# Kernel tuning notes

Hardware: AMD Instinct MI355X
Metric: run time of the kernel (lower is better)

The kernel has to match this reference:

```python
import jax, jax.numpy as jnp
import numpy as np

NUM_LAYERS = 3
NUM_NODES = 120000  # num_users + num_items
LATENT_DIM = 64
NUM_EDGES = 2000000


def setup_inputs() -> dict:
    key = jax.random.key(0)
    k1, k2 = jax.random.split(key)
    edge_index = jax.random.randint(k1, (2, NUM_EDGES), 0, NUM_NODES, dtype=jnp.int64 if jax.config.jax_enable_x64 else jnp.int32)
    # init_parameters: normal(std=0.1) for LightGCN
    emb_weight = jax.random.normal(k2, (NUM_NODES, LATENT_DIM), dtype=jnp.float32) * 0.1
    return {"edge_index": edge_index, "emb_weight": emb_weight}


def reference(edge_index, emb_weight):
    """RecSysGNN (model='LightGCN') forward. Returns (emb0, out)."""
    n = emb_weight.shape[0]
    src, dst = edge_index[0], edge_index[1]
    # degree of target nodes (degree(to_, x.size(0)))
    deg = jax.ops.segment_sum(jnp.ones(src.shape[0], dtype=emb_weight.dtype), dst, num_segments=n)
    deg_inv_sqrt = jnp.where(deg > 0, jax.lax.rsqrt(jnp.maximum(deg, 1.0)), 0.0)
    norm = deg_inv_sqrt[src] * deg_inv_sqrt[dst]  # [E]

    emb0 = emb_weight
    emb = emb0
    acc = emb0  # running sum of layer embeddings for final mean
    for _ in range(NUM_LAYERS):
        msg = norm[:, None] * emb[src]                      # [E, d] gather + scale
        emb = jax.ops.segment_sum(msg, dst, num_segments=n)  # scatter-add to targets
        acc = acc + emb
    out = acc / (NUM_LAYERS + 1)  # mean over stacked [emb0, emb1, ..., embL]
    return (emb0, out)
```

## Files before the change

kernel.cpp:

```cpp
#include <hip/hip_runtime.h>


#define DIM 64
#define BN 512
#define BSH 9
#define CHUNK 4096

typedef unsigned short u16;
typedef unsigned int u32;

static __device__ __forceinline__ float bf2f_lo(u32 p) { return __uint_as_float(p << 16); }
static __device__ __forceinline__ float bf2f_hi(u32 p) { return __uint_as_float(p & 0xffff0000u); }
static __device__ __forceinline__ u16 f2bf(float f) {
    unsigned u = __float_as_uint(f);
    return (u16)((u + 0x7fffu + ((u >> 16) & 1u)) >> 16);
}
static __device__ __forceinline__ u32 pack2(float a, float b) {
    return (u32)f2bf(a) | ((u32)f2bf(b) << 16);
}

__global__ void zero_cur(int* __restrict__ cursor) { cursor[threadIdx.x] = 0; }

__global__ void __launch_bounds__(512) c1_scatter(
        const int* __restrict__ src, const int* __restrict__ dst,
        int* __restrict__ cursor, u32* __restrict__ slab, int E, int CAP) {
    __shared__ u32 buf[CHUNK];
    __shared__ unsigned char bb[CHUNK];
    __shared__ int posb[256], startb[256], gbase[256];
    int w = blockIdx.x, tid = threadIdx.x;
    int lo = w * CHUNK, hi = min(lo + CHUNK, E);
    if (tid < 256) posb[tid] = 0;
    __syncthreads();
    for (int i = lo + tid; i < hi; i += 512) atomicAdd(&posb[dst[i] >> BSH], 1);
    __syncthreads();
    int x = 0;
    if (tid < 256) {
        x = posb[tid];
        gbase[tid] = x ? atomicAdd(cursor + tid, x) : 0;
    }
    __syncthreads();
    for (int off = 1; off < 256; off <<= 1) {
        int t = (tid >= off && tid < 256) ? posb[tid - off] : 0;
        __syncthreads();
        if (tid < 256) posb[tid] += t;
        __syncthreads();
    }
    if (tid < 256) startb[tid] = posb[tid] - x;
    __syncthreads();
    if (tid < 256) posb[tid] = startb[tid];
    __syncthreads();
    for (int i = lo + tid; i < hi; i += 512) {
        int d = dst[i], b = d >> BSH;
        int q = atomicAdd(&posb[b], 1);
        buf[q] = ((u32)src[i] << BSH) | (u32)(d & (BN - 1));
        bb[q] = (unsigned char)b;
    }
    __syncthreads();
    int n = hi - lo;
    for (int q = tid; q < n; q += 512) {
        int b = bb[q];
        slab[(size_t)b * CAP + gbase[b] + (q - startb[b])] = buf[q];
    }
}

__global__ void __launch_bounds__(512) c3_build(
        const u32* __restrict__ slab, const int* __restrict__ cursor,
        int* __restrict__ col, int2* __restrict__ row_se, float* __restrict__ dis,
        int N, int CAP, int NB) {
    __shared__ int cur[BN];
    __shared__ int ps[512];
    int b = blockIdx.x, tid = threadIdx.x;
    int xc = (tid < NB) ? cursor[tid] : 0;
    if (tid < 256) ps[tid] = xc;
    __syncthreads();
    for (int off = 1; off < 256; off <<= 1) {
        int t = (tid >= off && tid < 256) ? ps[tid - off] : 0;
        __syncthreads();
        if (tid < 256) ps[tid] += t;
        __syncthreads();
    }
    int lo  = b ? ps[b - 1] : 0;
    int cnt = cursor[b];
    __syncthreads();

    int nodeBase = b << BSH;
    int nLoc = min(BN, N - nodeBase);
    const u32* sp = slab + (size_t)b * CAP;
    cur[tid] = 0;
    __syncthreads();
    for (int i = tid; i < cnt; i += 512) atomicAdd(&cur[sp[i] & (BN - 1)], 1);
    __syncthreads();
    int c0 = cur[tid];
    ps[tid] = c0;
    __syncthreads();
    for (int off = 1; off < 512; off <<= 1) {
        int t = (tid >= off) ? ps[tid - off] : 0;
        __syncthreads();
        ps[tid] += t;
        __syncthreads();
    }
    int base = ps[tid] - c0;
    cur[tid] = base;
    if (tid < nLoc) {
        dis[nodeBase + tid] = c0 ? rsqrtf((float)c0) : 0.f;
        row_se[nodeBase + tid] = make_int2(lo + base, lo + base + c0);
    }
    __syncthreads();
    for (int i = tid; i < cnt; i += 512) {
        u32 v = sp[i];
        int q = atomicAdd(&cur[v & (BN - 1)], 1);
        col[lo + q] = (int)(v >> BSH);
    }
}

__global__ void cvt_copy(const float4* __restrict__ emb, const float* __restrict__ dis,
                         ushort4* __restrict__ e0b, float4* __restrict__ emb0_out, int n4) {
    int i = blockIdx.x * blockDim.x + threadIdx.x;
    if (i < n4) {
        float4 v = emb[i];
        float w = dis[i >> 4];
        ushort4 o;
        o.x = f2bf(w * v.x); o.y = f2bf(w * v.y);
        o.z = f2bf(w * v.z); o.w = f2bf(w * v.w);
        e0b[i] = o;
        emb0_out[i] = v;
    }
}

#define GATHER_BODY(CURTAB)                                                    \
    float s0 = 0.f, s1 = 0.f, s2 = 0.f, s3 = 0.f;                              \
    {                                                                          \
        int j = start;                                                         \
        for (; j + 8 <= end; j += 8) {                                         \
            _Pragma("unroll")                                                  \
            for (int k = 0; k < 4; ++k) {                                      \
                int c = col[j + 2 * k + g];                                    \
                uint2 p = *(const uint2*)((CURTAB) + (((size_t)c) << 5) + 2 * d); \
                s0 += bf2f_lo(p.x); s1 += bf2f_hi(p.x);                        \
                s2 += bf2f_lo(p.y); s3 += bf2f_hi(p.y);                        \
            }                                                                  \
        }                                                                      \
        if (j < end) {                                                         \
            int endm1 = end - 1;                                               \
            _Pragma("unroll")                                                  \
            for (int k = 0; k < 4; ++k) {                                      \
                int e = j + 2 * k + g;                                         \
                int c = col[min(e, endm1)];                                    \
                uint2 p = *(const uint2*)((CURTAB) + (((size_t)c) << 5) + 2 * d); \
                if (e >= end) { p.x = 0; p.y = 0; }                            \
                s0 += bf2f_lo(p.x); s1 += bf2f_hi(p.x);                        \
                s2 += bf2f_lo(p.y); s3 += bf2f_hi(p.y);                        \
            }                                                                  \
        }                                                                      \
    }                                                                          \
    s0 += __shfl_xor(s0, 16); s1 += __shfl_xor(s1, 16);                        \
    s2 += __shfl_xor(s2, 16); s3 += __shfl_xor(s3, 16);

__global__ void __launch_bounds__(256) gather_mid(
        const int2* __restrict__ row_se, const int* __restrict__ col,
        const float* __restrict__ dis, const u32* __restrict__ cur,
        u32* __restrict__ next, int N) {
    int t = blockIdx.x * blockDim.x + threadIdx.x;
    int pair = t >> 6, lane = t & 63;
    if (2 * pair >= N) return;
    int node = 2 * pair + (lane >> 5);
    int g = (lane >> 4) & 1, d = lane & 15;
    bool valid = node < N;
    int2 se = valid ? row_se[node] : make_int2(0, 0);
    int start = se.x, end = se.y;
    GATHER_BODY(cur)
    if (valid && g == 0) {
        float w = dis[node], ww = w * w;
        uint2 o;
        o.x = pack2(ww * s0, ww * s1);
        o.y = pack2(ww * s2, ww * s3);
        *(uint2*)(next + (((size_t)node) << 5) + 2 * d) = o;
    }
}

__global__ void __launch_bounds__(256) gather_final(
        const int2* __restrict__ row_se, const int* __restrict__ col,
        const float* __restrict__ dis, const u32* __restrict__ cur ,
        const u32* __restrict__ e1b, const float* __restrict__ emb0,
        float* __restrict__ out, int N) {
    int t = blockIdx.x * blockDim.x + threadIdx.x;
    int pair = t >> 6, lane = t & 63;
    if (2 * pair >= N) return;
    int node = 2 * pair + (lane >> 5);
    int g = (lane >> 4) & 1, d = lane & 15;
    bool valid = node < N;
    int2 se = valid ? row_se[node] : make_int2(0, 0);
    int start = se.x, end = se.y;
    GATHER_BODY(cur)
    if (valid && g == 0) {
        float w = dis[node];
        float inv = (w > 0.f) ? 1.0f / w : 0.f;
        size_t idx = (((size_t)node) << 5) + 2 * d;
        uint2 q1 = *(const uint2*)(e1b + idx);
        uint2 q2 = *(const uint2*)(cur + idx);
        float4 e0 = *(const float4*)(emb0 + 2 * idx);
        float4 r;
        r.x = 0.25f * (e0.x + (bf2f_lo(q1.x) + bf2f_lo(q2.x)) * inv + w * s0);
        r.y = 0.25f * (e0.y + (bf2f_hi(q1.x) + bf2f_hi(q2.x)) * inv + w * s1);
        r.z = 0.25f * (e0.z + (bf2f_lo(q1.y) + bf2f_lo(q2.y)) * inv + w * s2);
        r.w = 0.25f * (e0.w + (bf2f_hi(q1.y) + bf2f_hi(q2.y)) * inv + w * s3);
        *(float4*)(out + 2 * idx) = r;
    }
}

extern "C" void kernel_launch(void* const* d_in, const int* in_sizes, int n_in,
                              void* d_out, int out_size, void* d_ws, size_t ws_size,
                              hipStream_t stream) {
    const int*   edge  = (const int*)d_in[0];
    const float* emb_w = (const float*)d_in[1];
    const int E = in_sizes[0] / 2;
    const int N = in_sizes[1] / DIM;
    const int* src = edge;
    const int* dst = edge + E;

    const int NB  = (N + BN - 1) >> BSH;
    const int nCh = (E + CHUNK - 1) / CHUNK;
    const int CAP = (E / (NB > 0 ? NB : 1)) * 2;

    float* out_base = (float*)d_out;
    float* emb0_out = out_base;
    float* acc      = out_base + (size_t)N * DIM;

    float* dis       = (float*)d_ws;
    int2*  row_se    = (int2*)(dis + ((N + 1) & ~1));
    int*   cursor    = (int*)(row_se + N);
    int*   col       = cursor + 256;
    u32*   slab      = (u32*)(col + E);
    u16*   e0b       = (u16*)slab;
    u16*   e1b       = e0b + (size_t)N * DIM;

    const int n4    = N * DIM / 4;
    const int BLK   = 256;
    const int g4    = (n4 + BLK - 1) / BLK;
    const int PAIRS = (N + 1) / 2;
    const int gW    = (PAIRS * 64 + BLK - 1) / BLK;

    zero_cur<<<1, 256, 0, stream>>>(cursor);
    c1_scatter<<<nCh, 512, 0, stream>>>(src, dst, cursor, slab, E, CAP);
    c3_build<<<NB, 512, 0, stream>>>(slab, cursor, col, row_se, dis, N, CAP, NB);

    cvt_copy<<<g4, BLK, 0, stream>>>((const float4*)emb_w, dis,
                                     (ushort4*)e0b, (float4*)emb0_out, n4);

    gather_mid<<<gW, BLK, 0, stream>>>(row_se, col, dis, (const u32*)e0b, (u32*)e1b, N);
    gather_mid<<<gW, BLK, 0, stream>>>(row_se, col, dis, (const u32*)e1b, (u32*)e0b, N);
    gather_final<<<gW, BLK, 0, stream>>>(row_se, col, dis, (const u32*)e0b, (const u32*)e1b,
                                         emb_w, acc, N);
}
```

Before: 262.5 us.

## Split embedding table into four feature-quarter planes for cache-local gathers

Stores the bf16 scaled embeddings as four separate planes of 16 features each, and launches gather blocks per quarter so each pass touches only a quarter-sized table that fits better in cache. Each node now uses 8 lanes (two edge groups of 4 lanes) in place of 32, and the neighbor loop is rewritten as a software-pipelined wave-uniform loop that prefetches the next column index and row. This adds four times as many blocks and re-reads col/row_se per quarter, and each gather is now only 8 bytes per lane, in exchange for better L2 locality.

```diff
diff --git a/kernel.cpp b/kernel.cpp
--- a/kernel.cpp
+++ b/kernel.cpp
@@ -114,97 +114,97 @@
 }
 
 __global__ void cvt_copy(const float4* __restrict__ emb, const float* __restrict__ dis,
-                         ushort4* __restrict__ e0b, float4* __restrict__ emb0_out, int n4) {
+                         u32* __restrict__ e0bT, float4* __restrict__ emb0_out,
+                         int n4, int N) {
     int i = blockIdx.x * blockDim.x + threadIdx.x;
     if (i < n4) {
         float4 v = emb[i];
-        float w = dis[i >> 4];
-        ushort4 o;
-        o.x = f2bf(w * v.x); o.y = f2bf(w * v.y);
-        o.z = f2bf(w * v.z); o.w = f2bf(w * v.w);
-        e0b[i] = o;
+        int node = i >> 4;
+        int q    = (i >> 2) & 3;
+        int d4   = i & 3;
+        float w = dis[node];
+        uint2 o;
+        o.x = pack2(w * v.x, w * v.y);
+        o.y = pack2(w * v.z, w * v.w);
+        *(uint2*)(e0bT + ((size_t)q * N + node) * 8 + 2 * d4) = o;
         emb0_out[i] = v;
     }
 }
 
-#define GATHER_BODY(CURTAB)                                                    \
+#define GATHERQ_BODY(CURTAB)                                                   \
     float s0 = 0.f, s1 = 0.f, s2 = 0.f, s3 = 0.f;                              \
     {                                                                          \
-        int j = start;                                                         \
-        for (; j + 8 <= end; j += 8) {                                         \
-            _Pragma("unroll")                                                  \
-            for (int k = 0; k < 4; ++k) {                                      \
-                int c = col[j + 2 * k + g];                                    \
-                uint2 p = *(const uint2*)((CURTAB) + (((size_t)c) << 5) + 2 * d); \
-                s0 += bf2f_lo(p.x); s1 += bf2f_hi(p.x);                        \
-                s2 += bf2f_lo(p.y); s3 += bf2f_hi(p.y);                        \
-            }                                                                  \
-        }                                                                      \
-        if (j < end) {                                                         \
-            int endm1 = end - 1;                                               \
-            _Pragma("unroll")                                                  \
-            for (int k = 0; k < 4; ++k) {                                      \
-                int e = j + 2 * k + g;                                         \
-                int c = col[min(e, endm1)];                                    \
-                uint2 p = *(const uint2*)((CURTAB) + (((size_t)c) << 5) + 2 * d); \
-                if (e >= end) { p.x = 0; p.y = 0; }                            \
-                s0 += bf2f_lo(p.x); s1 += bf2f_hi(p.x);                        \
-                s2 += bf2f_lo(p.y); s3 += bf2f_hi(p.y);                        \
-            }                                                                  \
+        const u32* tq = (CURTAB) + ((size_t)q * N) * 8 + 2 * d4;               \
+        int Em1 = E - 1;                                                       \
+        int m = (end - start - g + 1) >> 1;                                    \
+        int e = start + g;                                                     \
+        u32 cA = col[min(e, Em1)];                                             \
+        u32 cB = col[min(e + 2, Em1)];                                         \
+        uint2 p = *(const uint2*)(tq + ((size_t)cA << 3));                     \
+        if (m <= 0) { p.x = 0; p.y = 0; }                                      \
+        int mm = m, ee = e + 4;                                                \
+        while (__any(mm > 0)) {                                                \
+            u32 cC = col[min(ee, Em1)];                                        \
+            uint2 pn = *(const uint2*)(tq + ((size_t)cB << 3));                \
+            if (mm <= 1) { pn.x = 0; pn.y = 0; }                               \
+            s0 += bf2f_lo(p.x); s1 += bf2f_hi(p.x);                            \
+            s2 += bf2f_lo(p.y); s3 += bf2f_hi(p.y);                            \
+            p = pn; cB = cC; --mm; ee += 2;                                    \
         }                                                                      \
     }                                                                          \
-    s0 += __shfl_xor(s0, 16); s1 += __shfl_xor(s1, 16);                        \
-    s2 += __shfl_xor(s2, 16); s3 += __shfl_xor(s3, 16);
-
-__global__ void __launch_bounds__(256) gather_mid(
+    s0 += __shfl_xor(s0, 4); s1 += __shfl_xor(s1, 4);                          \
+    s2 += __shfl_xor(s2, 4); s3 += __shfl_xor(s3, 4);
+
+__global__ void __launch_bounds__(256) gatherq_mid(
         const int2* __restrict__ row_se, const int* __restrict__ col,
         const float* __restrict__ dis, const u32* __restrict__ cur,
-        u32* __restrict__ next, int N) {
-    int t = blockIdx.x * blockDim.x + threadIdx.x;
-    int pair = t >> 6, lane = t & 63;
-    if (2 * pair >= N) return;
-    int node = 2 * pair + (lane >> 5);
-    int g = (lane >> 4) & 1, d = lane & 15;
-    bool valid = node < N;
-    int2 se = valid ? row_se[node] : make_int2(0, 0);
+        u32* __restrict__ next, int N, int E) {
+    int b = blockIdx.x, tid = threadIdx.x;
+    int q    = b & 3;
+    int node = (b >> 2) * 32 + (tid >> 3);
+    int g    = (tid >> 2) & 1;
+    int d4   = tid & 3;
+    bool vn  = node < N;
+    int2 se  = vn ? row_se[node] : make_int2(0, 0);
     int start = se.x, end = se.y;
-    GATHER_BODY(cur)
-    if (valid && g == 0) {
+    GATHERQ_BODY(cur)
+    if (vn && g == 0) {
         float w = dis[node], ww = w * w;
         uint2 o;
         o.x = pack2(ww * s0, ww * s1);
         o.y = pack2(ww * s2, ww * s3);
-        *(uint2*)(next + (((size_t)node) << 5) + 2 * d) = o;
-    }
-}
-
-__global__ void __launch_bounds__(256) gather_final(
+        *(uint2*)(next + ((size_t)q * N + node) * 8 + 2 * d4) = o;
+    }
+}
+
+__global__ void __launch_bounds__(256) gatherq_final(
         const int2* __restrict__ row_se, const int* __restrict__ col,
         const float* __restrict__ dis, const u32* __restrict__ cur ,
-        const u32* __restrict__ e1b, const float* __restrict__ emb0,
-        float* __restrict__ out, int N) {
-    int t = blockIdx.x * blockDim.x + threadIdx.x;
-    int pair = t >> 6, lane = t & 63;
-    if (2 * pair >= N) return;
-    int node = 2 * pair + (lane >> 5);
-    int g = (lane >> 4) & 1, d = lane & 15;
-    bool valid = node < N;
-    int2 se = valid ? row_se[node] : make_int2(0, 0);
+        const u32* __restrict__ e1b , const float* __restrict__ emb0,
+        float* __restrict__ out, int N, int E) {
+    int b = blockIdx.x, tid = threadIdx.x;
+    int q    = b & 3;
+    int node = (b >> 2) * 32 + (tid >> 3);
+    int g    = (tid >> 2) & 1;
+    int d4   = tid & 3;
+    bool vn  = node < N;
+    int2 se  = vn ? row_se[node] : make_int2(0, 0);
     int start = se.x, end = se.y;
-    GATHER_BODY(cur)
-    if (valid && g == 0) {
+    GATHERQ_BODY(cur)
+    if (vn && g == 0) {
         float w = dis[node];
         float inv = (w > 0.f) ? 1.0f / w : 0.f;
-        size_t idx = (((size_t)node) << 5) + 2 * d;
-        uint2 q1 = *(const uint2*)(e1b + idx);
-        uint2 q2 = *(const uint2*)(cur + idx);
-        float4 e0 = *(const float4*)(emb0 + 2 * idx);
+        size_t ti = ((size_t)q * N + node) * 8 + 2 * d4;
+        uint2 q1 = *(const uint2*)(e1b + ti);
+        uint2 q2 = *(const uint2*)(cur + ti);
+        size_t fo = (size_t)node * 64 + q * 16 + d4 * 4;
+        float4 e0 = *(const float4*)(emb0 + fo);
         float4 r;
         r.x = 0.25f * (e0.x + (bf2f_lo(q1.x) + bf2f_lo(q2.x)) * inv + w * s0);
         r.y = 0.25f * (e0.y + (bf2f_hi(q1.x) + bf2f_hi(q2.x)) * inv + w * s1);
         r.z = 0.25f * (e0.z + (bf2f_lo(q1.y) + bf2f_lo(q2.y)) * inv + w * s2);
         r.w = 0.25f * (e0.w + (bf2f_hi(q1.y) + bf2f_hi(q2.y)) * inv + w * s3);
-        *(float4*)(out + 2 * idx) = r;
+        *(float4*)(out + fo) = r;
     }
 }
 
@@ -231,24 +231,24 @@
     int*   cursor    = (int*)(row_se + N);
     int*   col       = cursor + 256;
     u32*   slab      = (u32*)(col + E);
-    u16*   e0b       = (u16*)slab;
-    u16*   e1b       = e0b + (size_t)N * DIM;
-
-    const int n4    = N * DIM / 4;
-    const int BLK   = 256;
-    const int g4    = (n4 + BLK - 1) / BLK;
-    const int PAIRS = (N + 1) / 2;
-    const int gW    = (PAIRS * 64 + BLK - 1) / BLK;
+    u32*   e0bT      = slab;
+    u32*   e1bT      = e0bT + (size_t)N * 32;
+
+    const int n4  = N * DIM / 4;
+    const int BLK = 256;
+    const int g4  = (n4 + BLK - 1) / BLK;
+    const int NBK = (N + 31) / 32;
+    const int gQ  = 4 * NBK;
 
     zero_cur<<<1, 256, 0, stream>>>(cursor);
     c1_scatter<<<nCh, 512, 0, stream>>>(src, dst, cursor, slab, E, CAP);
     c3_build<<<NB, 512, 0, stream>>>(slab, cursor, col, row_se, dis, N, CAP, NB);
 
     cvt_copy<<<g4, BLK, 0, stream>>>((const float4*)emb_w, dis,
-                                     (ushort4*)e0b, (float4*)emb0_out, n4);
-
-    gather_mid<<<gW, BLK, 0, stream>>>(row_se, col, dis, (const u32*)e0b, (u32*)e1b, N);
-    gather_mid<<<gW, BLK, 0, stream>>>(row_se, col, dis, (const u32*)e1b, (u32*)e0b, N);
-    gather_final<<<gW, BLK, 0, stream>>>(row_se, col, dis, (const u32*)e0b, (const u32*)e1b,
-                                         emb_w, acc, N);
-}
+                                     e0bT, (float4*)emb0_out, n4, N);
+
+    gatherq_mid<<<gQ, BLK, 0, stream>>>(row_se, col, dis, e0bT, e1bT, N, E);
+    gatherq_mid<<<gQ, BLK, 0, stream>>>(row_se, col, dis, e1bT, e0bT, N, E);
+    gatherq_final<<<gQ, BLK, 0, stream>>>(row_se, col, dis, e0bT, e1bT,
+                                          emb_w, acc, N, E);
+}
```

Result: slower. 404.3 us (+54.0%).
